# Optimization experiments

Hardware: AMD Instinct MI355X
Metric: run time of the kernel (lower is better)

Reference implementation:

```python
import jax, jax.numpy as jnp
import numpy as np

ALPHA = 0.2  # LeakyReLU negative slope
NEG_FILL = -9e15


def setup_inputs() -> dict:
    key = jax.random.key(0)
    k_adj, k_x, k_W, k_a = jax.random.split(key, 4)
    n, in_feats, out_feats = 12288, 256, 64
    adj = jax.random.randint(k_adj, (n, n), 0, 2, dtype=jnp.int32)
    x = jax.random.normal(k_x, (n, in_feats), dtype=jnp.float32)
    W = jax.random.normal(k_W, (in_feats, out_feats), dtype=jnp.float32) * 0.1
    a = jax.random.normal(k_a, (2 * out_feats, 1), dtype=jnp.float32) * 0.1
    return {"adj": adj, "x": x, "W": W, "a": a}


def reference(adj, x, W, a):
    out_feats = W.shape[1]
    h = x @ W                                  # (n, out_feats)
    wh1 = h @ a[:out_feats]                    # (n, 1)
    wh2 = h @ a[out_feats:]                    # (n, 1)
    e = jax.nn.leaky_relu(wh1 + wh2, ALPHA)    # (n, 1) -- faithful to source (no transpose)
    # broadcast (n,1) scores against (n,n) adjacency mask
    attention = jnp.where(adj > 0, e, NEG_FILL)
    attention = jax.nn.softmax(attention, axis=1)
    # dropout p=0.0 -> identity (eval mode)
    h_prime = attention @ h                    # (n, out_feats)
    return jax.nn.elu(h_prime)                 # concat=True
```

## Files before the change

kernel.cpp:

```cpp
#include <hip/hip_runtime.h>
#include <hip/hip_bf16.h>

#define N_NODES 12288
#define IN_F    256
#define OUT_F   64
#define KSPLIT  4
#define BK      64
#define MT      64

typedef __attribute__((ext_vector_type(8))) short bf16x8;
typedef __attribute__((ext_vector_type(4))) float f32x4;

__device__ __forceinline__ unsigned short f2bf(float f) {
    union { float f; unsigned int i; } v; v.f = f;
    unsigned int x = v.i;
    unsigned int r = x + 0x7FFFu + ((x >> 16) & 1u);
    return (unsigned short)(r >> 16);
}

__global__ __launch_bounds__(256) void k_h(const float* __restrict__ x,
                                           const float* __restrict__ W,
                                           unsigned short* __restrict__ h) {
    int lane = threadIdx.x & 63;
    int wave = threadIdx.x >> 6;
    int i = blockIdx.x * 4 + wave;
    const float* xr = x + (size_t)i * IN_F;
    float acc = 0.f;
    #pragma unroll 8
    for (int k = 0; k < IN_F; ++k) {
        acc = fmaf(xr[k], W[k * OUT_F + lane], acc);
    }
    h[(size_t)i * OUT_F + lane] = f2bf(acc);
}

__global__ __launch_bounds__(256) void k_t(const unsigned short* __restrict__ h,
                                           unsigned short* __restrict__ hT) {
    __shared__ unsigned short tl[64][65];
    int tid = threadIdx.x;
    int i0 = blockIdx.x * 64;
    int r  = tid >> 2;
    int cq = (tid & 3) * 16;
    #pragma unroll
    for (int u = 0; u < 16; ++u)
        tl[r][cq + u] = h[(size_t)(i0 + r) * OUT_F + cq + u];
    __syncthreads();
    #pragma unroll
    for (int u = 0; u < 16; ++u)
        hT[(size_t)r * N_NODES + i0 + cq + u] = tl[cq + u][r];
}

__global__ __launch_bounds__(256) void k_spmm(const int* __restrict__ adj,
                                              const unsigned short* __restrict__ hT,
                                              float* __restrict__ s_part,
                                              int* __restrict__ deg_part) {
    __shared__ __align__(16) unsigned short As[64][72];
    __shared__ __align__(16) unsigned short Bs[64][72];

    int tid  = threadIdx.x;
    int lane = tid & 63;
    int wave = tid >> 6;
    int q    = lane >> 4;
    int ml   = lane & 15;
    int i0   = blockIdx.x * MT;
    int ks   = blockIdx.y;
    int k0b  = ks * (N_NODES / KSPLIT);
    int r    = tid >> 2;
    int cq   = (tid & 3) * 16;

    f32x4 acc[4];
    #pragma unroll
    for (int nt = 0; nt < 4; ++nt) acc[nt] = (f32x4){0.f, 0.f, 0.f, 0.f};
    int degacc = 0;

    const int iters = (N_NODES / KSPLIT) / BK;
    for (int it = 0; it < iters; ++it) {
        int k0 = k0b + it * BK;

        const int* ap = adj + (size_t)(i0 + r) * N_NODES + k0 + cq;
        int4 a0 = ((const int4*)ap)[0];
        int4 a1 = ((const int4*)ap)[1];
        int4 a2 = ((const int4*)ap)[2];
        int4 a3 = ((const int4*)ap)[3];

        const unsigned short* bp = hT + (size_t)r * N_NODES + k0 + cq;
        uint4 b01 = ((const uint4*)bp)[0];
        uint4 b23 = ((const uint4*)bp)[1];

        degacc += a0.x + a0.y + a0.z + a0.w;
        degacc += a1.x + a1.y + a1.z + a1.w;
        degacc += a2.x + a2.y + a2.z + a2.w;
        degacc += a3.x + a3.y + a3.z + a3.w;

        ushort4 c0, c1, c2, c3;
        c0.x = a0.x ? 0x3F80 : 0; c0.y = a0.y ? 0x3F80 : 0; c0.z = a0.z ? 0x3F80 : 0; c0.w = a0.w ? 0x3F80 : 0;
        c1.x = a1.x ? 0x3F80 : 0; c1.y = a1.y ? 0x3F80 : 0; c1.z = a1.z ? 0x3F80 : 0; c1.w = a1.w ? 0x3F80 : 0;
        c2.x = a2.x ? 0x3F80 : 0; c2.y = a2.y ? 0x3F80 : 0; c2.z = a2.z ? 0x3F80 : 0; c2.w = a2.w ? 0x3F80 : 0;
        c3.x = a3.x ? 0x3F80 : 0; c3.y = a3.y ? 0x3F80 : 0; c3.z = a3.z ? 0x3F80 : 0; c3.w = a3.w ? 0x3F80 : 0;

        *(ushort4*)&As[r][cq + 0]  = c0;
        *(ushort4*)&As[r][cq + 4]  = c1;
        *(ushort4*)&As[r][cq + 8]  = c2;
        *(ushort4*)&As[r][cq + 12] = c3;
        *(uint4*)&Bs[r][cq + 0] = b01;
        *(uint4*)&Bs[r][cq + 8] = b23;

        __syncthreads();

        #pragma unroll
        for (int kk = 0; kk < BK; kk += 32) {
            bf16x8 av = *(const bf16x8*)&As[16 * wave + ml][kk + 8 * q];
            #pragma unroll
            for (int nt = 0; nt < 4; ++nt) {
                bf16x8 bv = *(const bf16x8*)&Bs[16 * nt + ml][kk + 8 * q];
                acc[nt] = __builtin_amdgcn_mfma_f32_16x16x32_bf16(av, bv, acc[nt], 0, 0, 0);
            }
        }

        __syncthreads();
    }

    float* sp = s_part + (size_t)ks * ((size_t)N_NODES * OUT_F);
    #pragma unroll
    for (int nt = 0; nt < 4; ++nt) {
        #pragma unroll
        for (int rr = 0; rr < 4; ++rr) {
            int row = i0 + 16 * wave + 4 * q + rr;
            int col = 16 * nt + ml;
            sp[(size_t)row * OUT_F + col] = acc[nt][rr];
        }
    }

    degacc += __shfl_xor(degacc, 1, 64);
    degacc += __shfl_xor(degacc, 2, 64);
    if ((tid & 3) == 0)
        deg_part[ks * N_NODES + i0 + r] = degacc;
}

__global__ __launch_bounds__(256) void k_out(const float* __restrict__ s_part,
                                             const int* __restrict__ deg_part,
                                             float* __restrict__ out) {
    int idx = blockIdx.x * 256 + threadIdx.x;
    int i = idx >> 6;
    float s = 0.f; int deg = 0;
    #pragma unroll
    for (int p = 0; p < KSPLIT; ++p) {
        s   += s_part[(size_t)p * ((size_t)N_NODES * OUT_F) + idx];
        deg += deg_part[p * N_NODES + i];
    }
    float v = (deg > 0) ? (s / (float)deg) : 0.f;
    float o = (v > 0.f) ? v : expm1f(v);
    out[idx] = o;
}

extern "C" void kernel_launch(void* const* d_in, const int* in_sizes, int n_in,
                              void* d_out, int out_size, void* d_ws, size_t ws_size,
                              hipStream_t stream) {
    const int*   adj = (const int*)d_in[0];
    const float* x   = (const float*)d_in[1];
    const float* W   = (const float*)d_in[2];
    float* out = (float*)d_out;

    char* ws = (char*)d_ws;
    const size_t h_bytes  = (size_t)N_NODES * OUT_F * 2;
    const size_t sp_bytes = (size_t)KSPLIT * N_NODES * OUT_F * 4;
    unsigned short* h  = (unsigned short*)ws;
    unsigned short* hT = (unsigned short*)(ws + h_bytes);
    float* s_part      = (float*)(ws + 2 * h_bytes);
    int*   deg_part    = (int*)(ws + 2 * h_bytes + sp_bytes);

    k_h   <<<dim3(N_NODES / 4),           dim3(256), 0, stream>>>(x, W, h);
    k_t   <<<dim3(N_NODES / 64),          dim3(256), 0, stream>>>(h, hT);
    k_spmm<<<dim3(N_NODES / MT, KSPLIT),  dim3(256), 0, stream>>>(adj, hT, s_part, deg_part);
    k_out <<<dim3(N_NODES * OUT_F / 256), dim3(256), 0, stream>>>(s_part, deg_part, out);
}
```

Before: 865.3 us.

## Fuse feature projection and transpose into one MFMA kernel writing hT

Replaces the scalar FMA projection kernel and the separate transpose kernel with one kernel. It computes x@W using bf16 MFMA, with W staged transposed in shared memory, and writes the transposed bf16 hT directly. This drops one launch, the round trip of h through global memory, and the slow scalar GEMM. In exchange, x and W are now rounded to bf16 before the matmul, which changes precision, and every block reloads and converts all of W.

```diff
diff --git a/kernel.cpp b/kernel.cpp
--- a/kernel.cpp
+++ b/kernel.cpp
@@ -1,5 +1,4 @@
 #include <hip/hip_runtime.h>
-#include <hip/hip_bf16.h>
 
 #define N_NODES 12288
 #define IN_F    256
@@ -18,35 +17,48 @@
     return (unsigned short)(r >> 16);
 }
 
-__global__ __launch_bounds__(256) void k_h(const float* __restrict__ x,
-                                           const float* __restrict__ W,
-                                           unsigned short* __restrict__ h) {
-    int lane = threadIdx.x & 63;
-    int wave = threadIdx.x >> 6;
-    int i = blockIdx.x * 4 + wave;
-    const float* xr = x + (size_t)i * IN_F;
-    float acc = 0.f;
-    #pragma unroll 8
-    for (int k = 0; k < IN_F; ++k) {
-        acc = fmaf(xr[k], W[k * OUT_F + lane], acc);
+__global__ __launch_bounds__(256) void k_hT(const float* __restrict__ x,
+                                            const float* __restrict__ W,
+                                            unsigned short* __restrict__ hT) {
+    __shared__ unsigned short WT[OUT_F][IN_F + 8];
+    int tid = threadIdx.x;
+    for (int idx = tid; idx < IN_F * OUT_F; idx += 256) {
+        int k = idx >> 6, n = idx & 63;
+        WT[n][k] = f2bf(W[idx]);
     }
-    h[(size_t)i * OUT_F + lane] = f2bf(acc);
-}
+    __syncthreads();
 
-__global__ __launch_bounds__(256) void k_t(const unsigned short* __restrict__ h,
-                                           unsigned short* __restrict__ hT) {
-    __shared__ unsigned short tl[64][65];
-    int tid = threadIdx.x;
-    int i0 = blockIdx.x * 64;
-    int r  = tid >> 2;
-    int cq = (tid & 3) * 16;
+    int lane = tid & 63, wave = tid >> 6;
+    int q = lane >> 4, ml = lane & 15;
+    int i0 = blockIdx.x * MT;
+    int row = i0 + 16 * wave + ml;
+    const float* xr = x + (size_t)row * IN_F + 8 * q;
+
+    f32x4 acc[4];
     #pragma unroll
-    for (int u = 0; u < 16; ++u)
-        tl[r][cq + u] = h[(size_t)(i0 + r) * OUT_F + cq + u];
-    __syncthreads();
+    for (int nt = 0; nt < 4; ++nt) acc[nt] = (f32x4){0.f, 0.f, 0.f, 0.f};
+
     #pragma unroll
-    for (int u = 0; u < 16; ++u)
-        hT[(size_t)r * N_NODES + i0 + cq + u] = tl[cq + u][r];
+    for (int kk = 0; kk < IN_F; kk += 32) {
+        float4 x0 = *(const float4*)(xr + kk);
+        float4 x1 = *(const float4*)(xr + kk + 4);
+        union { bf16x8 v; unsigned short u[8]; } A;
+        A.u[0] = f2bf(x0.x); A.u[1] = f2bf(x0.y); A.u[2] = f2bf(x0.z); A.u[3] = f2bf(x0.w);
+        A.u[4] = f2bf(x1.x); A.u[5] = f2bf(x1.y); A.u[6] = f2bf(x1.z); A.u[7] = f2bf(x1.w);
+        #pragma unroll
+        for (int nt = 0; nt < 4; ++nt) {
+            bf16x8 bv = *(const bf16x8*)&WT[16 * nt + ml][kk + 8 * q];
+            acc[nt] = __builtin_amdgcn_mfma_f32_16x16x32_bf16(A.v, bv, acc[nt], 0, 0, 0);
+        }
+    }
+
+    #pragma unroll
+    for (int nt = 0; nt < 4; ++nt) {
+        ushort4 o;
+        o.x = f2bf(acc[nt][0]); o.y = f2bf(acc[nt][1]);
+        o.z = f2bf(acc[nt][2]); o.w = f2bf(acc[nt][3]);
+        *(ushort4*)&hT[(size_t)(16 * nt + ml) * N_NODES + i0 + 16 * wave + 4 * q] = o;
+    }
 }
 
 __global__ __launch_bounds__(256) void k_spmm(const int* __restrict__ adj,
@@ -148,8 +160,7 @@
         deg += deg_part[p * N_NODES + i];
     }
     float v = (deg > 0) ? (s / (float)deg) : 0.f;
-    float o = (v > 0.f) ? v : expm1f(v);
-    out[idx] = o;
+    out[idx] = (v > 0.f) ? v : expm1f(v);
 }
 
 extern "C" void kernel_launch(void* const* d_in, const int* in_sizes, int n_in,
@@ -161,15 +172,13 @@
     float* out = (float*)d_out;
 
     char* ws = (char*)d_ws;
-    const size_t h_bytes  = (size_t)N_NODES * OUT_F * 2;
+    const size_t hT_bytes = (size_t)N_NODES * OUT_F * 2;
     const size_t sp_bytes = (size_t)KSPLIT * N_NODES * OUT_F * 4;
-    unsigned short* h  = (unsigned short*)ws;
-    unsigned short* hT = (unsigned short*)(ws + h_bytes);
-    float* s_part      = (float*)(ws + 2 * h_bytes);
-    int*   deg_part    = (int*)(ws + 2 * h_bytes + sp_bytes);
+    unsigned short* hT = (unsigned short*)ws;
+    float* s_part      = (float*)(ws + hT_bytes);
+    int*   deg_part    = (int*)(ws + hT_bytes + sp_bytes);
 
-    k_h   <<<dim3(N_NODES / 4),           dim3(256), 0, stream>>>(x, W, h);
-    k_t   <<<dim3(N_NODES / 64),          dim3(256), 0, stream>>>(h, hT);
+    k_hT  <<<dim3(N_NODES / MT),          dim3(256), 0, stream>>>(x, W, hT);
     k_spmm<<<dim3(N_NODES / MT, KSPLIT),  dim3(256), 0, stream>>>(adj, hT, s_part, deg_part);
     k_out <<<dim3(N_NODES * OUT_F / 256), dim3(256), 0, stream>>>(s_part, deg_part, out);
 }
```

After: 815.3 us. -5.8%, faster.
